# Performance work log

Measured on AMD Instinct MI355X. Metric: run time of the kernel, lower is better.

The kernel has to match this reference:

```python
import jax, jax.numpy as jnp
import numpy as np

N, E, D, H = 100000, 1600000, 32, 32


def setup_inputs() -> dict:
    key = jax.random.key(0)
    k1, k2, k3, k4 = jax.random.split(key, 4)
    x = jax.random.normal(k1, (N, D), dtype=jnp.float32)
    edge_index = jax.random.randint(k2, (2, E), 0, N, dtype=jnp.int64)
    W1 = jax.random.normal(k3, (D, H), dtype=jnp.float32) * (1.0 / np.sqrt(D))
    b1 = jnp.zeros((H,), dtype=jnp.float32)
    W2 = jax.random.normal(k4, (H, H), dtype=jnp.float32) * (1.0 / np.sqrt(H))
    b2 = jnp.zeros((H,), dtype=jnp.float32)
    return {"x": x, "edge_index": edge_index, "W1": W1, "b1": b1, "W2": W2, "b2": b2}


def _gcn_conv(x, src, dst, norm, W, b, n_nodes):
    # h = x W  ->  gather at src, scale by sym-norm, scatter-add at dst, + bias
    h = x @ W                                   # [N, H]
    msg = h[src] * norm[:, None]                # [E+N, H]
    out = jax.ops.segment_sum(msg, dst, num_segments=n_nodes)
    return out + b


def reference(x, edge_index, W1, b1, W2, b2):
    n = x.shape[0]
    loops = jnp.arange(n, dtype=edge_index.dtype)
    src = jnp.concatenate([edge_index[0], loops])  # source nodes (+ self loops)
    dst = jnp.concatenate([edge_index[1], loops])  # target nodes (+ self loops)
    # symmetric normalization: deg^{-1/2}[src] * deg^{-1/2}[dst] on A + I
    deg = jax.ops.segment_sum(jnp.ones_like(dst, dtype=x.dtype), dst, num_segments=n)
    dis = jnp.where(deg > 0, jax.lax.rsqrt(jnp.maximum(deg, 1e-12)), 0.0)
    norm = dis[src] * dis[dst]
    # layer 1: GCNConv -> ReLU (dropout is identity in eval mode)
    h = jax.nn.relu(_gcn_conv(x, src, dst, norm, W1, b1, n))
    # layer 2
    h = jax.nn.relu(_gcn_conv(h, src, dst, norm, W2, b2, n))
    return h
```

## Files before the change

kernel.cpp:

```cpp
#include <hip/hip_runtime.h>
#include <hip/hip_fp16.h>

#define FEAT 32
#define BIN_NODES 128
#define BIN_SHIFT 7
#define TILE_EDGES 8192
#define BWAVES 16
#define SRC_BITS 20
#define SRC_MASK 0xFFFFF

__device__ __forceinline__ int block_detect_int64(const int* __restrict__ raw32, int* nz) {
    if (threadIdx.x == 0) *nz = 0;
    __syncthreads();
    if (raw32[2 * threadIdx.x + 1] != 0) *nz = 1;
    __syncthreads();
    return (*nz == 0) ? 1 : 0;
}

__device__ __forceinline__ int load_idx(const void* raw, int f, long long i) {
    return f ? (int)((const long long*)raw)[i] : ((const int*)raw)[i];
}

__global__ __launch_bounds__(1024)
void binA_kernel(const void* __restrict__ raw, int* __restrict__ mat, int e, int nb) {
    extern __shared__ int hist[];
    int t = threadIdx.x;
    for (int i = t; i < BWAVES * nb; i += 1024) hist[i] = 0;
    int f = block_detect_int64((const int*)raw, &hist[BWAVES * nb]);
    int w = t >> 6, lane = t & 63;
    long long base = (long long)blockIdx.x * TILE_EDGES;
    int cnt = (int)min((long long)TILE_EDGES, (long long)e - base);
    int* hw = hist + w * nb;
    const int seg = TILE_EDGES / BWAVES;
    int wbeg = w * seg;
    int wend = min(wbeg + seg, cnt);
    for (int i = wbeg + lane; i < wend; i += 64) {
        int d = load_idx(raw, f, (long long)e + base + i);
        atomicAdd(&hw[d >> BIN_SHIFT], 1);
    }
    __syncthreads();
    for (int b = t; b < nb; b += 1024) {
        int s = 0;
#pragma unroll
        for (int w2 = 0; w2 < BWAVES; ++w2) s += hist[w2 * nb + b];
        mat[blockIdx.x * nb + b] = s;
    }
}

__device__ __forceinline__ int l2p(int L, int nb, int nblk) {
    int b = L / nblk;
    int k = L - b * nblk;
    return k * nb + b;
}

__global__ void scan1_kernel(int* __restrict__ mat, int* __restrict__ bsum,
                             int M, int nb, int nblk) {
    __shared__ int sd[256];
    int t = threadIdx.x;
    int L = blockIdx.x * 256 + t;
    int p = 0, v = 0;
    if (L < M) { p = l2p(L, nb, nblk); v = mat[p]; }
    sd[t] = v;
    __syncthreads();
    for (int off = 1; off < 256; off <<= 1) {
        int add = (t >= off) ? sd[t - off] : 0;
        __syncthreads();
        sd[t] += add;
        __syncthreads();
    }
    if (L < M) mat[p] = sd[t] - v;
    if (t == 255) bsum[blockIdx.x] = sd[t];
}

__global__ void scan2_kernel(int* __restrict__ bsum, int nbks) {
    __shared__ int sd[1024];
    int t = threadIdx.x;
    int v = (t < nbks) ? bsum[t] : 0;
    sd[t] = v;
    __syncthreads();
    for (int off = 1; off < 1024; off <<= 1) {
        int add = (t >= off) ? sd[t - off] : 0;
        __syncthreads();
        sd[t] += add;
        __syncthreads();
    }
    if (t < nbks) bsum[t] = sd[t] - v;
}

__global__ __launch_bounds__(1024)
void binC_kernel(const void* __restrict__ raw, const int* __restrict__ mat,
                 const int* __restrict__ bsum, int* __restrict__ packed,
                 int e, int nb, int nblk) {
    extern __shared__ int cur[];
    int t = threadIdx.x;
    int f = block_detect_int64((const int*)raw, &cur[nb]);
    for (int i = t; i < nb; i += 1024)
        cur[i] = mat[blockIdx.x * nb + i] + bsum[(i * nblk + blockIdx.x) >> 8];
    __syncthreads();
    long long base = (long long)blockIdx.x * TILE_EDGES;
    int cnt = (int)min((long long)TILE_EDGES, (long long)e - base);
    for (int i = t; i < cnt; i += 1024) {
        long long ei = base + i;
        int s = load_idx(raw, f, ei);
        int d = load_idx(raw, f, (long long)e + ei);
        int b = d >> BIN_SHIFT;
        int pos = atomicAdd(&cur[b], 1);
        packed[pos] = s | ((d & (BIN_NODES - 1)) << SRC_BITS);
    }
}

__global__ __launch_bounds__(1024)
void degsort_kernel(const int* __restrict__ packed, const int* __restrict__ mat,
                    const int* __restrict__ bsum, float* __restrict__ dis,
                    int* __restrict__ row_start, int* __restrict__ recs,
                    const float* __restrict__ x, const float* __restrict__ W1,
                    __half* __restrict__ h1,
                    int e, int n, int nb, int nblk) {
    __shared__ int cnt[BWAVES][BIN_NODES];
    __shared__ int wcur[BWAVES][BIN_NODES];
    __shared__ int exc[BIN_NODES];
    __shared__ float sdis[BIN_NODES];
    __shared__ float W1l[FEAT * FEAT];
    int b = blockIdx.x, t = threadIdx.x;
    int w = t >> 6;
    for (int i = t; i < BWAVES * BIN_NODES; i += 1024) ((int*)cnt)[i] = 0;
    if (t < FEAT * FEAT) W1l[t] = W1[t];
    __syncthreads();
    int start = mat[b] + bsum[(b * nblk) >> 8];
    int end = (b + 1 < nb) ? (mat[b + 1] + bsum[((b + 1) * nblk) >> 8]) : e;
    for (int i = start + t; i < end; i += 1024)
        atomicAdd(&cnt[w][packed[i] >> SRC_BITS], 1);
    __syncthreads();
    if (t < BIN_NODES) {
        int s = 0;
#pragma unroll
        for (int w2 = 0; w2 < BWAVES; ++w2) s += cnt[w2][t];
        exc[t] = s;
    }
    __syncthreads();
    for (int off = 1; off < BIN_NODES; off <<= 1) {
        int v = 0;
        if (t < BIN_NODES && t >= off) v = exc[t - off];
        __syncthreads();
        if (t < BIN_NODES) exc[t] += v;
        __syncthreads();
    }
    if (t < BIN_NODES) {
        int tot = 0;
#pragma unroll
        for (int w2 = 0; w2 < BWAVES; ++w2) tot += cnt[w2][t];
        int rs = start + exc[t] - tot;
        int run = rs;
#pragma unroll
        for (int w2 = 0; w2 < BWAVES; ++w2) { wcur[w2][t] = run; run += cnt[w2][t]; }
        float dv = rsqrtf((float)tot + 1.0f);
        sdis[t] = dv;
        int node = b * BIN_NODES + t;
        if (node < n) {
            dis[node] = dv;
            row_start[node] = rs;
        }
    }
    if (b == 0 && t == 128) row_start[n] = e;
    __syncthreads();
    for (int i = start + t; i < end; i += 1024) {
        int rec = packed[i];
        int pos = atomicAdd(&wcur[w][rec >> SRC_BITS], 1);
        recs[pos] = rec & SRC_MASK;
    }
    {
        int ln = b * BIN_NODES + (t >> 3);
        if (ln < n) {
            int q = t & 7;
            float4 xv = ((const float4*)x)[(size_t)ln * 8 + q];
            float xr[4] = {xv.x, xv.y, xv.z, xv.w};
            float o[4] = {0.f, 0.f, 0.f, 0.f};
#pragma unroll
            for (int k = 0; k < FEAT; ++k) {
                float xk = __shfl(xr[k & 3], k >> 2, 8);
#pragma unroll
                for (int c = 0; c < 4; ++c)
                    o[c] = fmaf(xk, W1l[k * FEAT + q * 4 + c], o[c]);
            }
            float dn = sdis[t >> 3];
            __half2* hp = (__half2*)&h1[(size_t)ln * FEAT + q * 4];
            hp[0] = __halves2half2(__float2half(dn * o[0]), __float2half(dn * o[1]));
            hp[1] = __halves2half2(__float2half(dn * o[2]), __float2half(dn * o[3]));
        }
    }
}

__global__ __launch_bounds__(256, 6)
void pull_mm_kernel(const int* __restrict__ recs, const int* __restrict__ row_start,
                    const __half* __restrict__ h, const float* __restrict__ dis,
                    const float* __restrict__ bias, const float* __restrict__ W2,
                    __half* __restrict__ h2, int n) {
    __shared__ float Wl[FEAT * FEAT];
    int t = threadIdx.x;
    for (int i = t; i < FEAT * FEAT; i += 256) Wl[i] = W2[i];
    __syncthreads();
    int node = blockIdx.x * 8 + (t >> 5);
    if (node >= n) return;
    int l32 = t & 31;
    int sub = l32 >> 2;
    int fb = l32 & 3;
    int start = row_start[node];
    int deg = row_start[node + 1] - start;
    const float4* h4 = (const float4*)h;
    float s0 = 0, s1 = 0, s2 = 0, s3 = 0, s4 = 0, s5 = 0, s6 = 0, s7 = 0;
    for (int r0 = 0; r0 < deg; r0 += 64) {
#pragma unroll
        for (int w = 0; w < 8; ++w) {
            int r = r0 + w * 8 + sub;
            if (r < deg) {
                int s = recs[start + r];
                float4 v = h4[(size_t)s * 4 + fb];
                const __half2* hp = (const __half2*)&v;
                float2 a = __half22float2(hp[0]);
                float2 b = __half22float2(hp[1]);
                float2 c = __half22float2(hp[2]);
                float2 d = __half22float2(hp[3]);
                s0 += a.x; s1 += a.y; s2 += b.x; s3 += b.y;
                s4 += c.x; s5 += c.y; s6 += d.x; s7 += d.y;
            }
        }
    }
#pragma unroll
    for (int m = 4; m <= 16; m <<= 1) {
        s0 += __shfl_xor(s0, m, 64); s1 += __shfl_xor(s1, m, 64);
        s2 += __shfl_xor(s2, m, 64); s3 += __shfl_xor(s3, m, 64);
        s4 += __shfl_xor(s4, m, 64); s5 += __shfl_xor(s5, m, 64);
        s6 += __shfl_xor(s6, m, 64); s7 += __shfl_xor(s7, m, 64);
    }
    float dn = dis[node];
    float4 hv = h4[(size_t)node * 4 + fb];
    const __half2* hp = (const __half2*)&hv;
    float2 a = __half22float2(hp[0]);
    float2 b = __half22float2(hp[1]);
    float2 c = __half22float2(hp[2]);
    float2 d = __half22float2(hp[3]);
    const float4* bv4 = (const float4*)bias;
    float4 b0 = bv4[fb * 2], b1 = bv4[fb * 2 + 1];
    float o[8];
    o[0] = fmaxf(fmaf(dn, s0 + a.x, b0.x), 0.0f);
    o[1] = fmaxf(fmaf(dn, s1 + a.y, b0.y), 0.0f);
    o[2] = fmaxf(fmaf(dn, s2 + b.x, b0.z), 0.0f);
    o[3] = fmaxf(fmaf(dn, s3 + b.y, b0.w), 0.0f);
    o[4] = fmaxf(fmaf(dn, s4 + c.x, b1.x), 0.0f);
    o[5] = fmaxf(fmaf(dn, s5 + c.y, b1.y), 0.0f);
    o[6] = fmaxf(fmaf(dn, s6 + d.x, b1.z), 0.0f);
    o[7] = fmaxf(fmaf(dn, s7 + d.y, b1.w), 0.0f);
    float acc = 0.0f;
#pragma unroll
    for (int k = 0; k < FEAT; ++k)
        acc = fmaf(__shfl(o[k & 7], k >> 3, 32), Wl[k * FEAT + l32], acc);
    h2[(size_t)node * FEAT + l32] = __float2half(dn * acc);
}

__global__ __launch_bounds__(256, 6)
void pull_kernel(const int* __restrict__ recs, const int* __restrict__ row_start,
                 const __half* __restrict__ h, const float* __restrict__ dis,
                 const float* __restrict__ bias, float* __restrict__ out,
                 int n, int relu_out) {
    int t = threadIdx.x;
    int node = blockIdx.x * 8 + (t >> 5);
    if (node >= n) return;
    int l32 = t & 31;
    int sub = l32 >> 2;
    int fb = l32 & 3;
    int start = row_start[node];
    int deg = row_start[node + 1] - start;
    const float4* h4 = (const float4*)h;
    float s0 = 0, s1 = 0, s2 = 0, s3 = 0, s4 = 0, s5 = 0, s6 = 0, s7 = 0;
    for (int r0 = 0; r0 < deg; r0 += 64) {
#pragma unroll
        for (int w = 0; w < 8; ++w) {
            int r = r0 + w * 8 + sub;
            if (r < deg) {
                int s = recs[start + r];
                float4 v = h4[(size_t)s * 4 + fb];
                const __half2* hp = (const __half2*)&v;
                float2 a = __half22float2(hp[0]);
                float2 b = __half22float2(hp[1]);
                float2 c = __half22float2(hp[2]);
                float2 d = __half22float2(hp[3]);
                s0 += a.x; s1 += a.y; s2 += b.x; s3 += b.y;
                s4 += c.x; s5 += c.y; s6 += d.x; s7 += d.y;
            }
        }
    }
#pragma unroll
    for (int m = 4; m <= 16; m <<= 1) {
        s0 += __shfl_xor(s0, m, 64); s1 += __shfl_xor(s1, m, 64);
        s2 += __shfl_xor(s2, m, 64); s3 += __shfl_xor(s3, m, 64);
        s4 += __shfl_xor(s4, m, 64); s5 += __shfl_xor(s5, m, 64);
        s6 += __shfl_xor(s6, m, 64); s7 += __shfl_xor(s7, m, 64);
    }
    if (sub == 0) {
        float dn = dis[node];
        float4 hv = h4[(size_t)node * 4 + fb];
        const __half2* hp = (const __half2*)&hv;
        float2 a = __half22float2(hp[0]);
        float2 b = __half22float2(hp[1]);
        float2 c = __half22float2(hp[2]);
        float2 d = __half22float2(hp[3]);
        const float4* bv4 = (const float4*)bias;
        float4 b0 = bv4[fb * 2], b1 = bv4[fb * 2 + 1];
        float4 o0, o1;
        o0.x = fmaf(dn, s0 + a.x, b0.x);
        o0.y = fmaf(dn, s1 + a.y, b0.y);
        o0.z = fmaf(dn, s2 + b.x, b0.z);
        o0.w = fmaf(dn, s3 + b.y, b0.w);
        o1.x = fmaf(dn, s4 + c.x, b1.x);
        o1.y = fmaf(dn, s5 + c.y, b1.y);
        o1.z = fmaf(dn, s6 + d.x, b1.z);
        o1.w = fmaf(dn, s7 + d.y, b1.w);
        if (relu_out) {
            o0.x = fmaxf(o0.x, 0.0f); o0.y = fmaxf(o0.y, 0.0f);
            o0.z = fmaxf(o0.z, 0.0f); o0.w = fmaxf(o0.w, 0.0f);
            o1.x = fmaxf(o1.x, 0.0f); o1.y = fmaxf(o1.y, 0.0f);
            o1.z = fmaxf(o1.z, 0.0f); o1.w = fmaxf(o1.w, 0.0f);
        }
        ((float4*)out)[(size_t)node * 8 + fb * 2] = o0;
        ((float4*)out)[(size_t)node * 8 + fb * 2 + 1] = o1;
    }
}

extern "C" void kernel_launch(void* const* d_in, const int* in_sizes, int n_in,
                              void* d_out, int out_size, void* d_ws, size_t ws_size,
                              hipStream_t stream) {
    const float* x = (const float*)d_in[0];
    const void* eidx_raw = d_in[1];
    const float* W1 = (const float*)d_in[2];
    const float* b1 = (const float*)d_in[3];
    const float* W2 = (const float*)d_in[4];
    const float* b2 = (const float*)d_in[5];
    float* out = (float*)d_out;

    const int n = in_sizes[0] / FEAT;
    const int e = in_sizes[1] / 2;
    const int nb = (n + BIN_NODES - 1) / BIN_NODES;
    const int nblk = (e + TILE_EDGES - 1) / TILE_EDGES;
    const int M = nb * nblk;
    const int nbks = (M + 255) / 256;

    char* ws = (char*)d_ws;
    size_t off = 0;
    auto alloc = [&](size_t bytes) { char* p = ws + off; off = (off + bytes + 255) & ~(size_t)255; return p; };
    int*    mat       = (int*)   alloc((size_t)M * 4);
    int*    bsum      = (int*)   alloc((size_t)nbks * 4);
    float*  dis       = (float*) alloc((size_t)n * 4);
    int*    row_start = (int*)   alloc((size_t)(n + 1) * 4);
    int*    recs      = (int*)   alloc((size_t)e * 4);
    __half* h1        = (__half*)alloc((size_t)n * FEAT * 2);
    __half* h2        = (__half*)alloc((size_t)(n * FEAT * 2 > e * 4 ? (size_t)n * FEAT * 2 : (size_t)e * 4));
    int*    packed    = (int*)h2;

    const size_t ldsA = (size_t)(BWAVES * nb + 1) * 4;
    const size_t ldsC = (size_t)(nb + 1) * 4;
    const int gNode = (n + 7) / 8;

    binA_kernel<<<nblk, 1024, ldsA, stream>>>(eidx_raw, mat, e, nb);
    scan1_kernel<<<nbks, 256, 0, stream>>>(mat, bsum, M, nb, nblk);
    scan2_kernel<<<1, 1024, 0, stream>>>(bsum, nbks);
    binC_kernel<<<nblk, 1024, ldsC, stream>>>(eidx_raw, mat, bsum, packed, e, nb, nblk);
    degsort_kernel<<<nb, 1024, 0, stream>>>(packed, mat, bsum, dis, row_start,
                                            recs, x, W1, h1, e, n, nb, nblk);

    pull_mm_kernel<<<gNode, 256, 0, stream>>>(recs, row_start, h1, dis, b1, W2, h2, n);
    pull_kernel<<<gNode, 256, 0, stream>>>(recs, row_start, h2, dis, b2, out, n, 1);
}
```

Before: 203.5 us.

## Use 16 lanes per node in pull kernels with swizzled-LDS partial matmul

Both pull kernels now give each node 16 lanes instead of 32, so a 256-thread block covers 16 nodes, with four edges gathered per pass and one fewer shuffle-reduction stage. In pull_mm the 32x32 W2 product is rebuilt: each lane multiplies its 8 aggregated features by an 8x8 block of W2 held in a bank-swizzled LDS layout, then partial sums are reduced across lanes and written as packed half vectors. The aim is less lane idling for low-degree nodes and fewer shuffles in the matmul, at the cost of less gather parallelism per node on high-degree rows. The relu_out flag is also dropped and ReLU applied unconditionally.

```diff
diff --git a/kernel.cpp b/kernel.cpp
--- a/kernel.cpp
+++ b/kernel.cpp
@@ -197,21 +197,25 @@
                     __half* __restrict__ h2, int n) {
     __shared__ float Wl[FEAT * FEAT];
     int t = threadIdx.x;
-    for (int i = t; i < FEAT * FEAT; i += 256) Wl[i] = W2[i];
-    __syncthreads();
-    int node = blockIdx.x * 8 + (t >> 5);
+    for (int i = t; i < FEAT * FEAT; i += 256) {
+        int k = i >> 5, j = i & 31;
+        int col = (j & 24) | ((j + 2 * (k >> 3)) & 7);
+        Wl[k * FEAT + col] = W2[i];
+    }
+    __syncthreads();
+    int node = blockIdx.x * 16 + (t >> 4);
     if (node >= n) return;
-    int l32 = t & 31;
-    int sub = l32 >> 2;
-    int fb = l32 & 3;
+    int g = t & 15;
+    int sub = g >> 2;
+    int fb = g & 3;
     int start = row_start[node];
     int deg = row_start[node + 1] - start;
     const float4* h4 = (const float4*)h;
     float s0 = 0, s1 = 0, s2 = 0, s3 = 0, s4 = 0, s5 = 0, s6 = 0, s7 = 0;
-    for (int r0 = 0; r0 < deg; r0 += 64) {
+    for (int r0 = 0; r0 < deg; r0 += 32) {
 #pragma unroll
         for (int w = 0; w < 8; ++w) {
-            int r = r0 + w * 8 + sub;
+            int r = r0 + w * 4 + sub;
             if (r < deg) {
                 int s = recs[start + r];
                 float4 v = h4[(size_t)s * 4 + fb];
@@ -226,7 +230,7 @@
         }
     }
 #pragma unroll
-    for (int m = 4; m <= 16; m <<= 1) {
+    for (int m = 4; m <= 8; m <<= 1) {
         s0 += __shfl_xor(s0, m, 64); s1 += __shfl_xor(s1, m, 64);
         s2 += __shfl_xor(s2, m, 64); s3 += __shfl_xor(s3, m, 64);
         s4 += __shfl_xor(s4, m, 64); s5 += __shfl_xor(s5, m, 64);
@@ -250,32 +254,51 @@
     o[5] = fmaxf(fmaf(dn, s5 + c.y, b1.y), 0.0f);
     o[6] = fmaxf(fmaf(dn, s6 + d.x, b1.z), 0.0f);
     o[7] = fmaxf(fmaf(dn, s7 + d.y, b1.w), 0.0f);
-    float acc = 0.0f;
-#pragma unroll
-    for (int k = 0; k < FEAT; ++k)
-        acc = fmaf(__shfl(o[k & 7], k >> 3, 32), Wl[k * FEAT + l32], acc);
-    h2[(size_t)node * FEAT + l32] = __float2half(dn * acc);
+    float part[8] = {0.f, 0.f, 0.f, 0.f, 0.f, 0.f, 0.f, 0.f};
+    const float* wrow = &Wl[(fb * 8) * FEAT + sub * 8];
+#pragma unroll
+    for (int cc = 0; cc < 8; ++cc) {
+#pragma unroll
+        for (int c2 = 0; c2 < 8; ++c2)
+            part[c2] = fmaf(o[cc], wrow[cc * FEAT + ((c2 + 2 * fb) & 7)], part[c2]);
+    }
+#pragma unroll
+    for (int m = 1; m <= 2; m <<= 1) {
+        part[0] += __shfl_xor(part[0], m, 64); part[1] += __shfl_xor(part[1], m, 64);
+        part[2] += __shfl_xor(part[2], m, 64); part[3] += __shfl_xor(part[3], m, 64);
+        part[4] += __shfl_xor(part[4], m, 64); part[5] += __shfl_xor(part[5], m, 64);
+        part[6] += __shfl_xor(part[6], m, 64); part[7] += __shfl_xor(part[7], m, 64);
+    }
+    if (fb == 0) {
+        __half2 p0 = __halves2half2(__float2half(dn * part[0]), __float2half(dn * part[1]));
+        __half2 p1 = __halves2half2(__float2half(dn * part[2]), __float2half(dn * part[3]));
+        __half2 p2 = __halves2half2(__float2half(dn * part[4]), __float2half(dn * part[5]));
+        __half2 p3 = __halves2half2(__float2half(dn * part[6]), __float2half(dn * part[7]));
+        float4 pk;
+        ((__half2*)&pk)[0] = p0; ((__half2*)&pk)[1] = p1;
+        ((__half2*)&pk)[2] = p2; ((__half2*)&pk)[3] = p3;
+        ((float4*)h2)[(size_t)node * 4 + sub] = pk;
+    }
 }
 
 __global__ __launch_bounds__(256, 6)
 void pull_kernel(const int* __restrict__ recs, const int* __restrict__ row_start,
                  const __half* __restrict__ h, const float* __restrict__ dis,
-                 const float* __restrict__ bias, float* __restrict__ out,
-                 int n, int relu_out) {
-    int t = threadIdx.x;
-    int node = blockIdx.x * 8 + (t >> 5);
+                 const float* __restrict__ bias, float* __restrict__ out, int n) {
+    int t = threadIdx.x;
+    int node = blockIdx.x * 16 + (t >> 4);
     if (node >= n) return;
-    int l32 = t & 31;
-    int sub = l32 >> 2;
-    int fb = l32 & 3;
+    int g = t & 15;
+    int sub = g >> 2;
+    int fb = g & 3;
     int start = row_start[node];
     int deg = row_start[node + 1] - start;
     const float4* h4 = (const float4*)h;
     float s0 = 0, s1 = 0, s2 = 0, s3 = 0, s4 = 0, s5 = 0, s6 = 0, s7 = 0;
-    for (int r0 = 0; r0 < deg; r0 += 64) {
+    for (int r0 = 0; r0 < deg; r0 += 32) {
 #pragma unroll
         for (int w = 0; w < 8; ++w) {
-            int r = r0 + w * 8 + sub;
+            int r = r0 + w * 4 + sub;
             if (r < deg) {
                 int s = recs[start + r];
                 float4 v = h4[(size_t)s * 4 + fb];
@@ -290,7 +313,7 @@
         }
     }
 #pragma unroll
-    for (int m = 4; m <= 16; m <<= 1) {
+    for (int m = 4; m <= 8; m <<= 1) {
         s0 += __shfl_xor(s0, m, 64); s1 += __shfl_xor(s1, m, 64);
         s2 += __shfl_xor(s2, m, 64); s3 += __shfl_xor(s3, m, 64);
         s4 += __shfl_xor(s4, m, 64); s5 += __shfl_xor(s5, m, 64);
@@ -307,20 +330,14 @@
         const float4* bv4 = (const float4*)bias;
         float4 b0 = bv4[fb * 2], b1 = bv4[fb * 2 + 1];
         float4 o0, o1;
-        o0.x = fmaf(dn, s0 + a.x, b0.x);
-        o0.y = fmaf(dn, s1 + a.y, b0.y);
-        o0.z = fmaf(dn, s2 + b.x, b0.z);
-        o0.w = fmaf(dn, s3 + b.y, b0.w);
-        o1.x = fmaf(dn, s4 + c.x, b1.x);
-        o1.y = fmaf(dn, s5 + c.y, b1.y);
-        o1.z = fmaf(dn, s6 + d.x, b1.z);
-        o1.w = fmaf(dn, s7 + d.y, b1.w);
-        if (relu_out) {
-            o0.x = fmaxf(o0.x, 0.0f); o0.y = fmaxf(o0.y, 0.0f);
-            o0.z = fmaxf(o0.z, 0.0f); o0.w = fmaxf(o0.w, 0.0f);
-            o1.x = fmaxf(o1.x, 0.0f); o1.y = fmaxf(o1.y, 0.0f);
-            o1.z = fmaxf(o1.z, 0.0f); o1.w = fmaxf(o1.w, 0.0f);
-        }
+        o0.x = fmaxf(fmaf(dn, s0 + a.x, b0.x), 0.0f);
+        o0.y = fmaxf(fmaf(dn, s1 + a.y, b0.y), 0.0f);
+        o0.z = fmaxf(fmaf(dn, s2 + b.x, b0.z), 0.0f);
+        o0.w = fmaxf(fmaf(dn, s3 + b.y, b0.w), 0.0f);
+        o1.x = fmaxf(fmaf(dn, s4 + c.x, b1.x), 0.0f);
+        o1.y = fmaxf(fmaf(dn, s5 + c.y, b1.y), 0.0f);
+        o1.z = fmaxf(fmaf(dn, s6 + d.x, b1.z), 0.0f);
+        o1.w = fmaxf(fmaf(dn, s7 + d.y, b1.w), 0.0f);
         ((float4*)out)[(size_t)node * 8 + fb * 2] = o0;
         ((float4*)out)[(size_t)node * 8 + fb * 2 + 1] = o1;
     }
@@ -358,7 +375,7 @@
 
     const size_t ldsA = (size_t)(BWAVES * nb + 1) * 4;
     const size_t ldsC = (size_t)(nb + 1) * 4;
-    const int gNode = (n + 7) / 8;
+    const int gNode = (n + 15) / 16;
 
     binA_kernel<<<nblk, 1024, ldsA, stream>>>(eidx_raw, mat, e, nb);
     scan1_kernel<<<nbks, 256, 0, stream>>>(mat, bsum, M, nb, nblk);
@@ -368,5 +385,5 @@
                                             recs, x, W1, h1, e, n, nb, nblk);
 
     pull_mm_kernel<<<gNode, 256, 0, stream>>>(recs, row_start, h1, dis, b1, W2, h2, n);
-    pull_kernel<<<gNode, 256, 0, stream>>>(recs, row_start, h2, dis, b2, out, n, 1);
-}
+    pull_kernel<<<gNode, 256, 0, stream>>>(recs, row_start, h2, dis, b2, out, n);
+}
```

After: 182.5 us. 10.3% less time.
